# Optimization experiments

Measured on AMD Instinct MI355X. Metric: run time of the kernel, lower is better.

## Reference

```python
import jax, jax.numpy as jnp
import numpy as np

LMAX=4; MMAX=2; L2=25; M2=19; C=64; CE=64; NRBF=600; CUT=5.0
HEADS=8; ACH=32; VCH=16; HMSG=64; HFF=128; G=288; NL=2
AVG_NEI=20.0; AVG_NODES=2000.0
N_NODES=2000; N_EDGES=40000; NSPEC=90
# |m| group of each truncated (edge-frame) coefficient, order l=0..4, m=-min(l,2)..min(l,2)
MG = np.array([0, 1,0,1, 2,1,0,1,2, 2,1,0,1,2, 2,1,0,1,2])
# l of each full SH coefficient (25 total)
LOC = np.array([0] + [1]*3 + [2]*5 + [3]*7 + [4]*9)

def silu(x):
    return x * jax.nn.sigmoid(x)

def rms_norm_sh(x, w):
    # x: [N, 25, C]; w: [5, C] per-degree affine weight (rms_norm_sh)
    ms = jnp.mean(x * x, axis=1, keepdims=True)
    return x * jax.lax.rsqrt(ms + 1e-6) * w[LOC][None]

def setup_inputs() -> dict:
    key = jax.random.key(0)
    ks = iter(jax.random.split(key, 64))
    def rn(shape, scale):
        return jax.random.normal(next(ks), shape, dtype=jnp.float32) * scale
    inp = {}
    inp['edge_vectors'] = rn((N_EDGES, 3), 1.5)
    inp['wigner'] = rn((N_EDGES, M2, L2), 0.2)
    inp['wigner_inv'] = rn((N_EDGES, L2, M2), 0.2)
    inp['species_embed'] = rn((NSPEC, C), 1.0)
    inp['edge_species_embed'] = rn((NSPEC, 2 * CE), 1.0)
    DIN = NRBF + 2 * CE  # 728
    inp['deg_W1'] = rn((DIN, 128), DIN ** -0.5)
    inp['deg_b1'] = jnp.zeros((128,), jnp.float32)
    inp['deg_W2'] = rn((128, M2 * C), 128 ** -0.5)
    inp['deg_b2'] = jnp.zeros((M2 * C,), jnp.float32)
    inp['norm1_w'] = jnp.ones((NL, 5, C), jnp.float32)
    inp['rad_W1'] = rn((NL, DIN, 128), DIN ** -0.5)
    inp['rad_b1'] = jnp.zeros((NL, 128), jnp.float32)
    inp['rad_W2'] = rn((NL, 128, 3 * 2 * C), 128 ** -0.5)
    inp['rad_b2'] = jnp.ones((NL, 3 * 2 * C), jnp.float32)
    inp['so2_W'] = rn((NL, 3, 2 * C, HMSG), (2 * C) ** -0.5)
    inp['alpha_W'] = rn((NL, HMSG, HEADS * ACH), HMSG ** -0.5)
    inp['alpha_vec'] = rn((NL, HEADS, ACH), ACH ** -0.5)
    inp['value_W'] = rn((NL, 3, HMSG, HEADS * VCH), HMSG ** -0.5)
    inp['proj_W'] = rn((NL, 3, HEADS * VCH, C), (HEADS * VCH) ** -0.5)
    inp['norm2_w'] = jnp.ones((NL, 5, C), jnp.float32)
    inp['ffn_W1'] = rn((NL, C, HFF), C ** -0.5)
    inp['ffn_b1'] = jnp.zeros((NL, HFF), jnp.float32)
    inp['ffn_W2'] = rn((NL, HFF, C), HFF ** -0.5)
    inp['to_grid'] = rn((G, L2), L2 ** -0.5)
    inp['from_grid'] = rn((L2, G), G ** -0.5)
    inp['final_norm_w'] = jnp.ones((5, C), jnp.float32)
    inp['en_W1'] = rn((C, HFF), C ** -0.5)
    inp['en_b1'] = jnp.zeros((HFF,), jnp.float32)
    inp['en_W2'] = rn((HFF, 1), HFF ** -0.5)
    inp['en_b2'] = jnp.zeros((1,), jnp.float32)
    inp['node_species'] = jax.random.randint(next(ks), (N_NODES,), 0, NSPEC, dtype=jnp.int32)
    inp['senders'] = jax.random.randint(next(ks), (N_EDGES,), 0, N_NODES, dtype=jnp.int32)
    inp['receivers'] = jax.random.randint(next(ks), (N_EDGES,), 0, N_NODES, dtype=jnp.int32)
    inp['n_node'] = jnp.array([N_NODES], jnp.int32)
    return inp

def reference(edge_vectors, wigner, wigner_inv, species_embed, edge_species_embed,
              deg_W1, deg_b1, deg_W2, deg_b2, norm1_w, rad_W1, rad_b1, rad_W2, rad_b2,
              so2_W, alpha_W, alpha_vec, value_W, proj_W, norm2_w, ffn_W1, ffn_b1, ffn_W2,
              to_grid, from_grid, final_norm_w, en_W1, en_b1, en_W2, en_b2,
              node_species, senders, receivers, n_node):
    N = node_species.shape[0]
    E = senders.shape[0]
    mg = jnp.asarray(MG)
    # Gaussian RBF distance expansion (rbf_width=2.0)
    d = jnp.sqrt(jnp.sum(edge_vectors * edge_vectors, axis=-1) + 1e-12)
    offs = jnp.linspace(0.0, CUT, NRBF)
    std = 2.0 * (CUT / (NRBF - 1))
    rbf = jnp.exp(-0.5 * ((d[:, None] - offs[None, :]) / std) ** 2)  # [E, 600]
    # shared atom-edge embedding concat
    ne = edge_species_embed[node_species]
    se, re = jnp.split(ne, 2, axis=-1)
    ee = jnp.concatenate([rbf, se[senders], re[receivers]], axis=1)  # [E, 728]
    # initial node features: species embedding on l=0 component
    x = jnp.zeros((N, L2, C), dtype=edge_vectors.dtype).at[:, 0, :].set(species_embed[node_species])
    # edge degree embedding: radial MLP -> edge-frame coeffs -> rotate back -> scatter
    h = silu(ee @ deg_W1 + deg_b1) @ deg_W2 + deg_b2
    deg = jnp.einsum('elm,emc->elc', wigner_inv, h.reshape(E, M2, C))  # [E,25,C]
    x = x + jax.ops.segment_sum(deg, receivers, num_segments=N) / AVG_NEI
    for i in range(NL):
        # --- SO2 equivariant graph attention ---
        res = x
        xn = rms_norm_sh(x, norm1_w[i])
        msg = jnp.concatenate([xn[senders], xn[receivers]], axis=-1)      # [E,25,2C]
        msg = jnp.einsum('eml,elc->emc', wigner, msg)                     # rotate to edge frame [E,19,2C]
        rad = (silu(ee @ rad_W1[i] + rad_b1[i]) @ rad_W2[i] + rad_b2[i]).reshape(E, MMAX + 1, 2 * C)
        msg = msg * rad[:, mg]                                            # per-|m| radial modulation
        h = jnp.einsum('emc,mco->emo', msg, so2_W[i][mg])                 # SO2 conv [E,19,HMSG]
        a = (silu(h[:, 0, :]) @ alpha_W[i]).reshape(E, HEADS, ACH)        # invariant (m=0) alpha path
        logits = jnp.sum(silu(a) * alpha_vec[i][None], axis=-1)           # [E,HEADS]
        mx = jax.ops.segment_max(logits, receivers, num_segments=N)[receivers]
        ex = jnp.exp(logits - mx)
        den = jax.ops.segment_sum(ex, receivers, num_segments=N)[receivers]
        attn = ex / (den + 1e-12)
        v = jnp.einsum('emo,mov->emv', h, value_W[i][mg]).reshape(E, M2, HEADS, VCH)
        v = (v * attn[:, None, :, None]).reshape(E, M2, HEADS * VCH)
        oe = jnp.einsum('emv,mvc->emc', v, proj_W[i][mg])                 # [E,19,C]
        oe = jnp.einsum('elm,emc->elc', wigner_inv, oe)                   # rotate back [E,25,C]
        x = res + jax.ops.segment_sum(oe, receivers, num_segments=N)
        # --- S2 grid feed-forward ---
        res = x
        xn = rms_norm_sh(x, norm2_w[i])
        g = jnp.einsum('gl,nlc->ngc', to_grid, xn)                        # [N,288,C]
        g = silu(g @ ffn_W1[i] + ffn_b1[i]) @ ffn_W2[i]
        x = res + jnp.einsum('lg,ngc->nlc', from_grid, g)
    # final norm + energy head
    xn = rms_norm_sh(x, final_norm_w)
    g = jnp.einsum('gl,nlc->ngc', to_grid, xn)
    g = silu(g @ en_W1 + en_b1) @ en_W2 + en_b2
    eo = jnp.einsum('lg,ngo->nlo', from_grid, g)
    return eo[:, 0, 0] / AVG_NODES
```

## Files before the change

kernel.cpp:

```cpp
#include <hip/hip_runtime.h>
#include <hip/hip_bf16.h>
#include <math.h>


#define NRBF 600
#define DIN 728
#define GPTS 288

typedef __attribute__((ext_vector_type(8))) short bf16x8;
typedef __attribute__((ext_vector_type(4))) float f32x4;

__constant__ int d_mg[19] = {0,1,0,1,2,1,0,1,2,2,1,0,1,2,2,1,0,1,2};
__constant__ int d_loc[25] = {0,1,1,1,2,2,2,2,2,3,3,3,3,3,3,3,4,4,4,4,4,4,4,4,4};
__constant__ int d_mg0[5]={0,2,6,11,16};
__constant__ int d_mg1[8]={1,3,5,7,10,12,15,17};
__constant__ int d_mg2[6]={4,8,9,13,14,18};

__device__ inline float silu_f(float v){ return v/(1.0f+__expf(-v)); }
__device__ inline float bf2f(unsigned short u){ return __uint_as_float(((unsigned)u)<<16); }
__device__ inline unsigned short f2bf(float f){
  unsigned b=__float_as_uint(f);
  return (unsigned short)((b + 0x7FFF + ((b>>16)&1)) >> 16);
}

__device__ inline void atomicMaxF(float* addr, float val){
  int* ia=(int*)addr;
  int old=*ia;
  while (__int_as_float(old) < val){
    int assumed=old;
    old = atomicCAS(ia, assumed, __float_as_int(val));
    if (old == assumed) break;
  }
}

__global__ __launch_bounds__(256) void zero_cnt_kernel(int* cnt, int N){
  int i = blockIdx.x*256+threadIdx.x;
  if (i<N) cnt[i]=0;
}
__global__ __launch_bounds__(256) void csr_count_kernel(const int* __restrict__ rcv, int* cnt, int E){
  int i = blockIdx.x*256+threadIdx.x;
  if (i<E) atomicAdd(&cnt[rcv[i]],1);
}
__global__ __launch_bounds__(256) void csr_scan_kernel(const int* __restrict__ cnt,
    int* rowptr, int* fill, int N){
  __shared__ int s_part[256];
  int tid=threadIdx.x;
  int chunk=(N+255)/256;
  int lvals[12];
  int base=tid*chunk;
  int lsum=0;
  for (int i=0;i<chunk && i<12;i++){
    int v=(base+i<N)?cnt[base+i]:0;
    lvals[i]=lsum; lsum+=v;
  }
  s_part[tid]=lsum;
  __syncthreads();
  if (tid==0){
    int run=0;
    for (int t=0;t<256;t++){ int v=s_part[t]; s_part[t]=run; run+=v; }
  }
  __syncthreads();
  int off=s_part[tid];
  for (int i=0;i<chunk && i<12;i++){
    if (base+i<N){ rowptr[base+i]=off+lvals[i]; fill[base+i]=off+lvals[i]; }
  }
  if (tid==255) rowptr[N]=off+lsum;
}
__global__ __launch_bounds__(256) void csr_fill_kernel(const int* __restrict__ rcv,
    int* fill, int* eix, int E){
  int i = blockIdx.x*256+threadIdx.x;
  if (i<E){ int p=atomicAdd(&fill[rcv[i]],1); eix[p]=i; }
}

__global__ __launch_bounds__(256) void wsvb_kernel(const float* __restrict__ so2W,
    const float* __restrict__ valW, unsigned short* __restrict__ wsvb){
  int i=blockIdx.x/3, g=blockIdx.x%3;
  const float* A = so2W + (size_t)i*24576 + g*8192;
  const float* B = valW + (size_t)i*24576 + g*8192;
  unsigned short* C = wsvb + (size_t)blockIdx.x*16384;
  __shared__ float sB[8192];
  for (int j=threadIdx.x;j<2048;j+=256) ((float4*)sB)[j]=((const float4*)B)[j];
  __syncthreads();
  for (int idx=threadIdx.x; idx<16384; idx+=256){
    int k=idx>>7, j=idx&127;
    float acc=0;
    #pragma unroll 4
    for (int o=0;o<64;o++) acc += A[k*64+o]*sB[o*128+j];
    int pos = ((k>>5)*8 + (j>>4))*512 + (((k>>3)&3)*16 + (j&15))*8 + (k&7);
    C[pos]=f2bf(acc);
  }
}

__global__ __launch_bounds__(256) void projb_kernel(const float* __restrict__ pW,
    unsigned short* __restrict__ projb){
  const float* src = pW + (size_t)blockIdx.x*8192;
  unsigned short* dst = projb + (size_t)blockIdx.x*8192;
  for (int idx=threadIdx.x; idx<8192; idx+=256){
    int k=idx>>6, j=idx&63;
    int pos = ((k>>5)*4 + (j>>4))*512 + (((k>>3)&3)*16 + (j&15))*8 + (k&7);
    dst[pos]=f2bf(src[idx]);
  }
}

__global__ __launch_bounds__(256) void packB2g_kernel(const float* __restrict__ src,
    unsigned short* __restrict__ dh, unsigned short* __restrict__ dl, int K, int Nn){
  int ktiles=(K+31)>>5;
  int nnt=Nn>>4;
  int tot=ktiles*nnt*512;
  for (int idx=blockIdx.x*256+threadIdx.x; idx<tot; idx+=gridDim.x*256){
    int f=idx>>9, r=idx&511, lane=r>>3, j=r&7;
    int kt=f/nnt, nt=f-kt*nnt;
    int k=kt*32+(lane>>4)*8+j, c=nt*16+(lane&15);
    float v=(k<K)? src[k*Nn+c] : 0.0f;
    unsigned short h=f2bf(v);
    dh[idx]=h;
    dl[idx]=f2bf(v-bf2f(h));
  }
}

__global__ __launch_bounds__(256) void pack_tg2_kernel(const float* __restrict__ tg,
    unsigned short* __restrict__ tgp){
  int tid=threadIdx.x;
  for (int idx=tid; idx<9216; idx+=256){
    int t=idx>>9, r=idx&511, lane=r>>3, j=r&7;
    int kl=(lane>>4)*8+j, row=t*16+(lane&15);
    float v=(kl<25)? tg[row*25+kl] : 0.0f;
    unsigned short h=f2bf(v);
    tgp[idx]=h;
    tgp[9216+idx]=f2bf(v-bf2f(h));
  }
}

__global__ __launch_bounds__(256) void pack_fg2_kernel(const float* __restrict__ fg,
    unsigned short* __restrict__ fgp){
  int tid=threadIdx.x;
  for (int idx=tid; idx<18432; idx+=256){
    int f=idx>>9, r=idx&511, lane=r>>3, j=r&7;
    int t=f>>1, mt=f&1;
    int row=mt*16+(lane&15), k=(lane>>4)*8+j;
    float v=(row<25 && k<16)? fg[row*288+t*16+k] : 0.0f;
    unsigned short h=f2bf(v);
    fgp[idx]=h;
    fgp[18432+idx]=f2bf(v-bf2f(h));
  }
}

__global__ __launch_bounds__(256) void mlp_edge_kernel(const float* __restrict__ ev,
    const float* __restrict__ ese, const int* __restrict__ nsp,
    const unsigned short* __restrict__ w1h, const unsigned short* __restrict__ w1l,
    const float* __restrict__ b1,
    const unsigned short* __restrict__ w2h, const unsigned short* __restrict__ w2l,
    const float* __restrict__ b2,
    const int* __restrict__ snd, const int* __restrict__ rcv, const int* __restrict__ eix,
    int use_eix, int nt2, int mode,
    unsigned short* __restrict__ outb, float* __restrict__ outf, int E){
  int tid=threadIdx.x, wv=tid>>6, lane=tid&63;
  int lanelo=lane&15, khi=lane>>4;
  int p0=blockIdx.x*16;
  __shared__ unsigned short s_eeh[11776], s_eel[11776];
  __shared__ unsigned short s_h1h[2048], s_h1l[2048];
  __shared__ float s_d[16]; __shared__ int s_ss[16], s_rs[16];
  if (tid<16){
    int p=p0+tid;
    int e=(p<E)? (use_eix? eix[p] : p) : -1;
    if (e>=0){
      float vx=ev[3*e], vy=ev[3*e+1], vz=ev[3*e+2];
      s_d[tid]=sqrtf(vx*vx+vy*vy+vz*vz+1e-12f);
      s_ss[tid]=nsp[snd[e]]; s_rs[tid]=nsp[rcv[e]];
    } else { s_d[tid]=0.0f; s_ss[tid]=0; s_rs[tid]=0; }
  }
  __syncthreads();
  const float step=5.0f/599.0f, inv_std=1.0f/(2.0f*step);
  for (int idx=tid; idx<11776; idx+=256){
    int f=idx>>9, r=idx&511, ln=r>>3, j=r&7;
    int k=f*32+((ln>>4)<<3)+j, row=ln&15;
    float v=0.0f;
    if (k<NRBF){ float t=(s_d[row]-k*step)*inv_std; v=__expf(-0.5f*t*t); }
    else if (k<NRBF+64) v=ese[s_ss[row]*128+(k-NRBF)];
    else if (k<DIN)     v=ese[s_rs[row]*128+64+(k-NRBF-64)];
    unsigned short h=f2bf(v);
    s_eeh[idx]=h; s_eel[idx]=f2bf(v-bf2f(h));
  }
  __syncthreads();
  {
    f32x4 acc0={0,0,0,0}, acc1={0,0,0,0};
    int nta=wv*2, ntb=nta+1;
    for (int kt=0;kt<23;kt++){
      bf16x8 Ah=*(const bf16x8*)(s_eeh + kt*512 + lane*8);
      bf16x8 Al=*(const bf16x8*)(s_eel + kt*512 + lane*8);
      const unsigned short* bpa=w1h+(size_t)(kt*8+nta)*512+lane*8;
      const unsigned short* bpl=w1l+(size_t)(kt*8+nta)*512+lane*8;
      bf16x8 Bh=*(const bf16x8*)bpa;
      bf16x8 Bl=*(const bf16x8*)bpl;
      acc0=__builtin_amdgcn_mfma_f32_16x16x32_bf16(Ah,Bh,acc0,0,0,0);
      acc0=__builtin_amdgcn_mfma_f32_16x16x32_bf16(Al,Bh,acc0,0,0,0);
      acc0=__builtin_amdgcn_mfma_f32_16x16x32_bf16(Ah,Bl,acc0,0,0,0);
      bf16x8 Bh2=*(const bf16x8*)(bpa+512);
      bf16x8 Bl2=*(const bf16x8*)(bpl+512);
      acc1=__builtin_amdgcn_mfma_f32_16x16x32_bf16(Ah,Bh2,acc1,0,0,0);
      acc1=__builtin_amdgcn_mfma_f32_16x16x32_bf16(Al,Bh2,acc1,0,0,0);
      acc1=__builtin_amdgcn_mfma_f32_16x16x32_bf16(Ah,Bl2,acc1,0,0,0);
    }
    #pragma unroll
    for (int q=0;q<4;q++){
      int row=khi*4+q;
      {
        int col=nta*16+lanelo;
        float v=silu_f(acc0[q]+b1[col]);
        int pos=row*128 + (((col>>3)^(row&7))<<3) + (col&7);
        unsigned short h=f2bf(v);
        s_h1h[pos]=h; s_h1l[pos]=f2bf(v-bf2f(h));
      }
      {
        int col=ntb*16+lanelo;
        float v=silu_f(acc1[q]+b1[col]);
        int pos=row*128 + (((col>>3)^(row&7))<<3) + (col&7);
        unsigned short h=f2bf(v);
        s_h1h[pos]=h; s_h1l[pos]=f2bf(v-bf2f(h));
      }
    }
  }
  __syncthreads();
  bf16x8 Ahh[4],Ahl[4];
  #pragma unroll
  for (int kt=0;kt<4;kt++){
    int o=lanelo*128 + (((kt*4+khi)^(lanelo&7))<<3);
    Ahh[kt]=*(const bf16x8*)(s_h1h+o);
    Ahl[kt]=*(const bf16x8*)(s_h1l+o);
  }
  int ostride=nt2*16;
  for (int nt=wv; nt<nt2; nt+=4){
    f32x4 acc={0,0,0,0};
    #pragma unroll
    for (int kt=0;kt<4;kt++){
      const unsigned short* bp=w2h+(size_t)(kt*nt2+nt)*512+lane*8;
      bf16x8 Bh=*(const bf16x8*)bp;
      bf16x8 Bl=*(const bf16x8*)(w2l+(size_t)(kt*nt2+nt)*512+lane*8);
      acc=__builtin_amdgcn_mfma_f32_16x16x32_bf16(Ahh[kt],Bh,acc,0,0,0);
      acc=__builtin_amdgcn_mfma_f32_16x16x32_bf16(Ahl[kt],Bh,acc,0,0,0);
      acc=__builtin_amdgcn_mfma_f32_16x16x32_bf16(Ahh[kt],Bl,acc,0,0,0);
    }
    int col=nt*16+lanelo;
    float bb=b2[col];
    #pragma unroll
    for (int q=0;q<4;q++){
      int p=p0+khi*4+q;
      if (p<E){
        if (mode==0) outb[(size_t)p*ostride+col]=f2bf(acc[q]+bb);
        else         outf[(size_t)p*ostride+col]=acc[q]+bb;
      }
    }
  }
}

__global__ __launch_bounds__(256) void deg_sum_kernel(const unsigned short* __restrict__ h2,
    const float* __restrict__ winv, const int* __restrict__ rowptr, const int* __restrict__ eix,
    const int* __restrict__ nsp, const float* __restrict__ spe,
    float* __restrict__ x, int N){
  int n=blockIdx.x, tid=threadIdx.x;
  __shared__ float s_winv[475];
  __shared__ unsigned short s_oe[1216];
  int row0=rowptr[n];
  int cnt=rowptr[n+1]-row0;
  float4 acc0={0,0,0,0}, acc1={0,0,0,0};
  int it1=tid+256;
  for (int j=0;j<cnt;j++){
    int p=row0+j;
    int e=eix[p];
    for (int k2=tid;k2<475;k2+=256) s_winv[k2]=winv[(size_t)e*475+k2];
    for (int k2=tid;k2<152;k2+=256) ((int4*)s_oe)[k2]=((const int4*)(h2+(size_t)p*1216))[k2];
    __syncthreads();
    const unsigned* o2=(const unsigned*)s_oe;
    {
      int l=tid>>4, c4=tid&15;
      const float* wr=s_winv+l*19;
      #pragma unroll
      for (int m=0;m<19;m++){
        float w=wr[m];
        unsigned ua=o2[m*32+c4*2], ub=o2[m*32+c4*2+1];
        acc0.x+=w*bf2f((unsigned short)(ua&0xffffu));
        acc0.y+=w*bf2f((unsigned short)(ua>>16));
        acc0.z+=w*bf2f((unsigned short)(ub&0xffffu));
        acc0.w+=w*bf2f((unsigned short)(ub>>16));
      }
    }
    if (it1<400){
      int l=it1>>4, c4=it1&15;
      const float* wr=s_winv+l*19;
      #pragma unroll
      for (int m=0;m<19;m++){
        float w=wr[m];
        unsigned ua=o2[m*32+c4*2], ub=o2[m*32+c4*2+1];
        acc1.x+=w*bf2f((unsigned short)(ua&0xffffu));
        acc1.y+=w*bf2f((unsigned short)(ua>>16));
        acc1.z+=w*bf2f((unsigned short)(ub&0xffffu));
        acc1.w+=w*bf2f((unsigned short)(ub>>16));
      }
    }
    __syncthreads();
  }
  int sp=nsp[n];
  const float4* sp4=(const float4*)(spe+(size_t)sp*64);
  float4* xp=(float4*)(x+(size_t)n*1600);
  {
    int l=tid>>4, c4=tid&15;
    float4 base=(l==0)? sp4[c4] : make_float4(0,0,0,0);
    float4 o;
    o.x=base.x+0.05f*acc0.x; o.y=base.y+0.05f*acc0.y;
    o.z=base.z+0.05f*acc0.z; o.w=base.w+0.05f*acc0.w;
    xp[tid]=o;
  }
  if (it1<400){
    float4 o;
    o.x=0.05f*acc1.x; o.y=0.05f*acc1.y; o.z=0.05f*acc1.z; o.w=0.05f*acc1.w;
    xp[it1]=o;
  }
}

__global__ __launch_bounds__(256) void rmsnorm_kernel(const float* __restrict__ x,
    const float* __restrict__ w, float* __restrict__ xn, int N){
  int n = blockIdx.x, tid = threadIdx.x;
  __shared__ float s_x[1600];
  __shared__ float s_part[256];
  __shared__ float s_ms[64];
  const float* xr = x + (size_t)n*1600;
  for (int j=tid;j<1600;j+=256) s_x[j]=xr[j];
  __syncthreads();
  {
    int c = tid&63, seg = tid>>6;
    float acc=0;
    for (int l=seg;l<25;l+=4){ float v=s_x[l*64+c]; acc+=v*v; }
    s_part[tid]=acc;
  }
  __syncthreads();
  if (tid<64){
    float m=(s_part[tid]+s_part[tid+64]+s_part[tid+128]+s_part[tid+192])*(1.0f/25.0f);
    s_ms[tid]=rsqrtf(m+1e-6f);
  }
  __syncthreads();
  float* xo = xn + (size_t)n*1600;
  for (int j=tid;j<1600;j+=256){
    int l=j>>6, c=j&63;
    xo[j]=s_x[j]*s_ms[c]*w[d_loc[l]*64+c];
  }
}

__global__ __launch_bounds__(256) void init_mxden_kernel(float* mx, float* den, int N){
  int idx = blockIdx.x*256+threadIdx.x;
  if (idx < N*8){ mx[idx]=-3.0e38f; den[idx]=0.0f; }
}

__global__ __launch_bounds__(256) void logits_kernel(const float* __restrict__ xn,
    const float* __restrict__ wig, const float* __restrict__ radb,
    const float* __restrict__ so2W, const float* __restrict__ alphaW, const float* __restrict__ alphaV,
    const int* __restrict__ snd, const int* __restrict__ rcv,
    float* __restrict__ logits, float* __restrict__ mx, int E){
  int e = blockIdx.x, tid = threadIdx.x;
  __shared__ float s_cat[3200];
  __shared__ float s_wig0[25];
  __shared__ float s_msg0[128];
  __shared__ float s_sh0[64];
  __shared__ float s_a[256];
  int s = snd[e], r = rcv[e];
  const float4* xs4 = (const float4*)(xn + (size_t)s*1600);
  const float4* xr4 = (const float4*)(xn + (size_t)r*1600);
  float4* cat4 = (float4*)s_cat;
  for (int j=tid;j<400;j+=256){
    int l=j>>4, c4=j&15;
    cat4[l*32+c4]    = xs4[j];
    cat4[l*32+16+c4] = xr4[j];
  }
  if (tid<25) s_wig0[tid]=wig[(size_t)e*475+tid];
  __syncthreads();
  if (tid<128){
    float acc=0;
    #pragma unroll
    for (int l=0;l<25;l++) acc += s_wig0[l]*s_cat[l*128+tid];
    s_msg0[tid]=acc*radb[(size_t)e*384+tid];
  }
  __syncthreads();
  if (tid<64){
    float acc=0;
    #pragma unroll
    for (int k=0;k<128;k++) acc += s_msg0[k]*so2W[k*64+tid];
    s_sh0[tid]=silu_f(acc);
  }
  __syncthreads();
  {
    float acc=0;
    #pragma unroll
    for (int o=0;o<64;o++) acc += s_sh0[o]*alphaW[o*256+tid];
    s_a[tid]=silu_f(acc)*alphaV[tid];
  }
  __syncthreads();
  if (tid<8){
    float lg=0;
    #pragma unroll
    for (int q=0;q<32;q++) lg += s_a[tid*32+q];
    logits[(size_t)e*8+tid]=lg;
    atomicMaxF(&mx[r*8+tid], lg);
  }
}

__global__ __launch_bounds__(256) void den_kernel(const float* __restrict__ logits,
    const float* __restrict__ mx, const int* __restrict__ rcv,
    float* __restrict__ den, int E){
  int idx = blockIdx.x*256+threadIdx.x;
  if (idx >= E*8) return;
  int e = idx>>3, hd = idx&7, r = rcv[e];
  atomicAdd(&den[r*8+hd], __expf(logits[idx]-mx[r*8+hd]));
}

__global__ __launch_bounds__(256) void msg_kernel(const float* __restrict__ xn,
    const float* __restrict__ wig, const float* __restrict__ radb,
    const int* __restrict__ snd, const int* __restrict__ rcv, const int* __restrict__ eix,
    unsigned short* __restrict__ msgb, int E){
  __shared__ float s_wig[1900];
  int tid=threadIdx.x, wv=tid>>6, lane=tid&63;
  int p=blockIdx.x*4+wv;
  bool act=(p<E);
  int pc=act? p : (E-1);
  int e=eix[pc];
  int node=(lane<32)? snd[e] : rcv[e];
  int c2=(lane&31)*2;
  int col0=c2+((lane>>5)<<6);
  const float* xb=xn+(size_t)node*1600+c2;
  float ca[25], cb[25];
  #pragma unroll
  for (int l=0;l<25;l++){
    float2 v=*(const float2*)(xb+l*64);
    ca[l]=v.x; cb[l]=v.y;
  }
  float* swig=s_wig+wv*475;
  for (int j=lane;j<475;j+=64) swig[j]=wig[(size_t)e*475+j];
  float ra0,ra1,rb0,rb1,rc0,rc1;
  {
    const float* rb_=radb+(size_t)e*384;
    float2 v0=*(const float2*)(rb_+col0);
    float2 v1=*(const float2*)(rb_+128+col0);
    float2 v2=*(const float2*)(rb_+256+col0);
    ra0=v0.x; ra1=v0.y; rb0=v1.x; rb1=v1.y; rc0=v2.x; rc1=v2.y;
  }
  __syncthreads();
  unsigned short* dst=msgb+(size_t)pc*2432+col0;
  constexpr int mgc[19]={0,1,0,1,2,1,0,1,2,2,1,0,1,2,2,1,0,1,2};
  if (act){
    #pragma unroll
    for (int m=0;m<19;m++){
      float a0=0.0f,a1=0.0f;
      const float* wr=swig+m*25;
      #pragma unroll
      for (int l=0;l<25;l++){ float w=wr[l]; a0+=w*ca[l]; a1+=w*cb[l]; }
      float r0,r1;
      if (mgc[m]==0){ r0=ra0; r1=ra1; }
      else if (mgc[m]==1){ r0=rb0; r1=rb1; }
      else { r0=rc0; r1=rc1; }
      a0*=r0; a1*=r1;
      unsigned packv=((unsigned)f2bf(a1)<<16)|(unsigned)f2bf(a0);
      *(unsigned*)(dst+m*128)=packv;
    }
  }
}

__global__ __launch_bounds__(256) void attn_gemm_kernel(unsigned short* __restrict__ msgb,
    const unsigned short* __restrict__ wsvp, const unsigned short* __restrict__ projp,
    const float* __restrict__ logits, const float* __restrict__ mx, const float* __restrict__ den,
    const int* __restrict__ eix, const int* __restrict__ rcv, int E){
  int tid=threadIdx.x, wv=tid>>6, lane=tid&63;
  int lanelo=lane&15, khi=lane>>4;
  int p0=blockIdx.x*16;
  __shared__ unsigned short s_vv[2176];
  __shared__ float s_attn[16][8];
  __shared__ short s_r2e[304], s_r2m[304];
  for (int j=tid;j<304;j+=256){
    int e,m;
    if (j<80){ e=j/5; m=d_mg0[j%5]; }
    else if (j<208){ int q=j-80; e=q>>3; m=d_mg1[q&7]; }
    else { int q=j-208; e=q/6; m=d_mg2[q%6]; }
    s_r2e[j]=(short)e; s_r2m[j]=(short)m;
  }
  if (tid<128){
    int i=tid>>3, h=tid&7, p=p0+i;
    float a=0.0f;
    if (p<E){
      int e=eix[p]; int r=rcv[e];
      a=__expf(logits[(size_t)e*8+h]-mx[r*8+h])/(den[r*8+h]+1e-12f);
    }
    s_attn[i][h]=a;
  }
  __syncthreads();
  const int4* wp4=(const int4*)wsvp;
  const int4* pp4=(const int4*)projp;
  for (int t=0;t<19;t++){
    int g=(t<5)?0:((t<13)?1:2);
    int R=t*16+lanelo;
    int ei=s_r2e[R], mi=s_r2m[R];
    int pp=p0+ei;
    size_t abase=((size_t)((pp<E)?pp:0))*2432 + (size_t)mi*128;
    bf16x8 A[4];
    #pragma unroll
    for (int kt=0;kt<4;kt++)
      A[kt]=*(const bf16x8*)(msgb + abase + kt*32 + khi*8);
    #pragma unroll
    for (int h2=0;h2<2;h2++){
      int nt=wv*2+h2;
      f32x4 acc={0,0,0,0};
      #pragma unroll
      for (int kt=0;kt<4;kt++){
        int4 tt=wp4[g*2048+(kt*8+nt)*64+lane];
        acc=__builtin_amdgcn_mfma_f32_16x16x32_bf16(A[kt],*(bf16x8*)&tt,acc,0,0,0);
      }
      int col=nt*16+lanelo;
      #pragma unroll
      for (int q=0;q<4;q++){
        int r16=khi*4+q;
        int ei2=s_r2e[t*16+r16];
        s_vv[r16*136+col]=f2bf(acc[q]*s_attn[ei2][nt]);
      }
    }
    __syncthreads();
    {
      bf16x8 A2[4];
      #pragma unroll
      for (int kt=0;kt<4;kt++)
        A2[kt]=*(const bf16x8*)(s_vv + lanelo*136 + kt*32 + khi*8);
      f32x4 acc={0,0,0,0};
      #pragma unroll
      for (int kt=0;kt<4;kt++){
        int4 tt=pp4[g*1024+(kt*4+wv)*64+lane];
        acc=__builtin_amdgcn_mfma_f32_16x16x32_bf16(A2[kt],*(bf16x8*)&tt,acc,0,0,0);
      }
      int col=wv*16+lanelo;
      #pragma unroll
      for (int q=0;q<4;q++){
        int R2=t*16+khi*4+q;
        int pi=p0+s_r2e[R2];
        if (pi<E) msgb[(size_t)pi*2432 + (size_t)s_r2m[R2]*128 + col]=f2bf(acc[q]);
      }
    }
    __syncthreads();
  }
}

__global__ __launch_bounds__(256) void attn_sum_kernel(const unsigned short* __restrict__ msgb,
    const float* __restrict__ winv, const int* __restrict__ rowptr, const int* __restrict__ eix,
    float* __restrict__ x, int N){
  int n=blockIdx.x, tid=threadIdx.x;
  __shared__ float s_winv[475];
  __shared__ unsigned short s_oe[1216];
  int row0=rowptr[n];
  int cnt=rowptr[n+1]-row0;
  float4 acc0={0,0,0,0}, acc1={0,0,0,0};
  int it1=tid+256;
  for (int j=0;j<cnt;j++){
    int p=row0+j;
    int e=eix[p];
    for (int k2=tid;k2<475;k2+=256) s_winv[k2]=winv[(size_t)e*475+k2];
    for (int k2=tid;k2<152;k2+=256){
      int m=k2>>3, jj=k2&7;
      ((int4*)s_oe)[k2]=*(const int4*)(msgb + (size_t)p*2432 + m*128 + jj*8);
    }
    __syncthreads();
    const unsigned* o2=(const unsigned*)s_oe;
    {
      int l=tid>>4, c4=tid&15;
      const float* wr=s_winv+l*19;
      #pragma unroll
      for (int m=0;m<19;m++){
        float w=wr[m];
        unsigned ua=o2[m*32+c4*2], ub=o2[m*32+c4*2+1];
        acc0.x+=w*bf2f((unsigned short)(ua&0xffffu));
        acc0.y+=w*bf2f((unsigned short)(ua>>16));
        acc0.z+=w*bf2f((unsigned short)(ub&0xffffu));
        acc0.w+=w*bf2f((unsigned short)(ub>>16));
      }
    }
    if (it1<400){
      int l=it1>>4, c4=it1&15;
      const float* wr=s_winv+l*19;
      #pragma unroll
      for (int m=0;m<19;m++){
        float w=wr[m];
        unsigned ua=o2[m*32+c4*2], ub=o2[m*32+c4*2+1];
        acc1.x+=w*bf2f((unsigned short)(ua&0xffffu));
        acc1.y+=w*bf2f((unsigned short)(ua>>16));
        acc1.z+=w*bf2f((unsigned short)(ub&0xffffu));
        acc1.w+=w*bf2f((unsigned short)(ub>>16));
      }
    }
    __syncthreads();
  }
  float4* xp=(float4*)(x+(size_t)n*1600);
  {
    float4 c=xp[tid];
    c.x+=acc0.x; c.y+=acc0.y; c.z+=acc0.z; c.w+=acc0.w;
    xp[tid]=c;
  }
  if (it1<400){
    float4 c=xp[it1];
    c.x+=acc1.x; c.y+=acc1.y; c.z+=acc1.z; c.w+=acc1.w;
    xp[it1]=c;
  }
}

__global__ __launch_bounds__(256) void grid_ffn_mfma_kernel(const float* __restrict__ xn,
    const unsigned short* __restrict__ tgp, const unsigned short* __restrict__ fgp,
    const unsigned short* __restrict__ w1p, const unsigned short* __restrict__ w2p,
    const float* __restrict__ b1, float* __restrict__ x, int N){
  int n=blockIdx.x, tid=threadIdx.x, wv=tid>>6, lane=tid&63;
  int lanelo=lane&15, khi=lane>>4;
  __shared__ __align__(16) char s_mem[74240];
  unsigned short* s_w1=(unsigned short*)s_mem;
  unsigned short* s_xn=(unsigned short*)(s_mem+32768);
  float* s_b1=(float*)(s_mem+40960);
  unsigned short* scr=(unsigned short*)(s_mem+41472)+(size_t)wv*4096;
  for (int j=tid;j<2048;j+=256) ((int4*)s_w1)[j]=((const int4*)w1p)[j];
  if (tid<128) s_b1[tid]=b1[tid];
  { int4 z={0,0,0,0}; for (int j=tid;j<512;j+=256) ((int4*)s_xn)[j]=z; }
  __syncthreads();
  {
    const float* xr=xn+(size_t)n*1600;
    for (int j=tid;j<1600;j+=256){
      int k=j>>6, c=j&63;
      float v=xr[j];
      unsigned short h=f2bf(v);
      s_xn[c*32+k]=h;
      s_xn[2048+c*32+k]=f2bf(v-bf2f(h));
    }
  }
  __syncthreads();
  bf16x8 XBh[4],XBl[4];
  #pragma unroll
  for (int ct=0;ct<4;ct++){
    int o=(ct*16+lanelo)*32 + khi*8;
    XBh[ct]=*(const bf16x8*)(s_xn+o);
    XBl[ct]=*(const bf16x8*)(s_xn+2048+o);
  }
  f32x4 oacc[2][4];
  #pragma unroll
  for (int mt=0;mt<2;mt++)
    #pragma unroll
    for (int nt=0;nt<4;nt++){ f32x4 z={0,0,0,0}; oacc[mt][nt]=z; }
  for (int t=wv;t<18;t+=4){
    bf16x8 Atgh=*(const bf16x8*)(tgp + t*512 + lane*8);
    bf16x8 Atgl=*(const bf16x8*)(tgp + 9216 + t*512 + lane*8);
    #pragma unroll
    for (int ct=0;ct<4;ct++){
      f32x4 g={0,0,0,0};
      g=__builtin_amdgcn_mfma_f32_16x16x32_bf16(Atgh,XBh[ct],g,0,0,0);
      g=__builtin_amdgcn_mfma_f32_16x16x32_bf16(Atgl,XBh[ct],g,0,0,0);
      g=__builtin_amdgcn_mfma_f32_16x16x32_bf16(Atgh,XBl[ct],g,0,0,0);
      #pragma unroll
      for (int q=0;q<4;q++){
        int row=khi*4+q, col=ct*16+lanelo;
        int pos=row*64 + (((col>>3)^(row&7))<<3) + (col&7);
        float v=g[q]; unsigned short h=f2bf(v);
        scr[pos]=h; scr[1024+pos]=f2bf(v-bf2f(h));
      }
    }
    bf16x8 Agh[2],Agl[2];
    #pragma unroll
    for (int kt=0;kt<2;kt++){
      int o=lanelo*64 + (((kt*4+khi)^(lanelo&7))<<3);
      Agh[kt]=*(const bf16x8*)(scr+o);
      Agl[kt]=*(const bf16x8*)(scr+1024+o);
    }
    #pragma unroll
    for (int nt=0;nt<8;nt++){
      f32x4 h={0,0,0,0};
      #pragma unroll
      for (int kt=0;kt<2;kt++){
        bf16x8 Bh=*(const bf16x8*)(s_w1 + (kt*8+nt)*512 + lane*8);
        bf16x8 Bl=*(const bf16x8*)(s_w1 + 8192 + (kt*8+nt)*512 + lane*8);
        h=__builtin_amdgcn_mfma_f32_16x16x32_bf16(Agh[kt],Bh,h,0,0,0);
        h=__builtin_amdgcn_mfma_f32_16x16x32_bf16(Agl[kt],Bh,h,0,0,0);
        h=__builtin_amdgcn_mfma_f32_16x16x32_bf16(Agh[kt],Bl,h,0,0,0);
      }
      #pragma unroll
      for (int q=0;q<4;q++){
        int row=khi*4+q, col=nt*16+lanelo;
        float v=silu_f(h[q]+s_b1[col]);
        int pos=row*128 + (((col>>3)^(row&7))<<3) + (col&7);
        unsigned short hh=f2bf(v);
        scr[pos]=hh; scr[2048+pos]=f2bf(v-bf2f(hh));
      }
    }
    bf16x8 Ahh[4],Ahl[4];
    #pragma unroll
    for (int kt=0;kt<4;kt++){
      int o=lanelo*128 + (((kt*4+khi)^(lanelo&7))<<3);
      Ahh[kt]=*(const bf16x8*)(scr+o);
      Ahl[kt]=*(const bf16x8*)(scr+2048+o);
    }
    #pragma unroll
    for (int nt=0;nt<4;nt++){
      f32x4 o4={0,0,0,0};
      #pragma unroll
      for (int kt=0;kt<4;kt++){
        bf16x8 Bh=*(const bf16x8*)(w2p + (kt*4+nt)*512 + lane*8);
        bf16x8 Bl=*(const bf16x8*)(w2p + 8192 + (kt*4+nt)*512 + lane*8);
        o4=__builtin_amdgcn_mfma_f32_16x16x32_bf16(Ahh[kt],Bh,o4,0,0,0);
        o4=__builtin_amdgcn_mfma_f32_16x16x32_bf16(Ahl[kt],Bh,o4,0,0,0);
        o4=__builtin_amdgcn_mfma_f32_16x16x32_bf16(Ahh[kt],Bl,o4,0,0,0);
      }
      #pragma unroll
      for (int q=0;q<4;q++){
        int ch=nt*16+lanelo, rowk=khi*4+q;
        int pos=ch*32 + (((rowk>>3)^(ch&3))<<3) + (rowk&7);
        float v=o4[q]; unsigned short hh=f2bf(v);
        scr[pos]=hh; scr[2048+pos]=f2bf(v-bf2f(hh));
      }
    }
    bf16x8 Boh[4],Bol[4];
    #pragma unroll
    for (int nt=0;nt<4;nt++){
      int ch=nt*16+lanelo;
      int o=ch*32 + ((khi^(ch&3))<<3);
      Boh[nt]=*(const bf16x8*)(scr+o);
      Bol[nt]=*(const bf16x8*)(scr+2048+o);
    }
    #pragma unroll
    for (int mt=0;mt<2;mt++){
      bf16x8 Afh=*(const bf16x8*)(fgp + (t*2+mt)*512 + lane*8);
      bf16x8 Afl=*(const bf16x8*)(fgp + 18432 + (t*2+mt)*512 + lane*8);
      #pragma unroll
      for (int nt=0;nt<4;nt++){
        oacc[mt][nt]=__builtin_amdgcn_mfma_f32_16x16x32_bf16(Afh,Boh[nt],oacc[mt][nt],0,0,0);
        oacc[mt][nt]=__builtin_amdgcn_mfma_f32_16x16x32_bf16(Afl,Boh[nt],oacc[mt][nt],0,0,0);
        oacc[mt][nt]=__builtin_amdgcn_mfma_f32_16x16x32_bf16(Afh,Bol[nt],oacc[mt][nt],0,0,0);
      }
    }
  }
  __syncthreads();
  float* pout=(float*)s_mem;
  #pragma unroll
  for (int mt=0;mt<2;mt++)
    #pragma unroll
    for (int nt=0;nt<4;nt++)
      #pragma unroll
      for (int q=0;q<4;q++){
        int row=mt*16+khi*4+q, col=nt*16+lanelo;
        pout[wv*2048 + row*64 + col]=oacc[mt][nt][q];
      }
  __syncthreads();
  for (int j=tid;j<1600;j+=256)
    x[(size_t)n*1600+j] += pout[j]+pout[2048+j]+pout[4096+j]+pout[6144+j];
}

__global__ __launch_bounds__(256) void energy_mfma_kernel(const float* __restrict__ xn,
    const unsigned short* __restrict__ tgp, const float* __restrict__ fg,
    const unsigned short* __restrict__ enw1p, const float* __restrict__ b1,
    const float* __restrict__ w2, const float* __restrict__ b2,
    float* __restrict__ out, int N){
  int n=blockIdx.x, tid=threadIdx.x, wv=tid>>6, lane=tid&63;
  int lanelo=lane&15, khi=lane>>4;
  __shared__ __align__(16) char s_mem[59584];
  unsigned short* s_w1=(unsigned short*)s_mem;
  unsigned short* s_xn=(unsigned short*)(s_mem+32768);
  float* s_b1=(float*)(s_mem+40960);
  float* s_w2=(float*)(s_mem+41472);
  float* s_fg0=(float*)(s_mem+41984);
  float* s_red=(float*)(s_mem+43136);
  unsigned short* scr=(unsigned short*)(s_mem+43200)+(size_t)wv*2048;
  for (int j=tid;j<2048;j+=256) ((int4*)s_w1)[j]=((const int4*)enw1p)[j];
  if (tid<128){ s_b1[tid]=b1[tid]; s_w2[tid]=w2[tid]; }
  for (int j=tid;j<288;j+=256) s_fg0[j]=fg[j];
  { int4 z={0,0,0,0}; for (int j=tid;j<512;j+=256) ((int4*)s_xn)[j]=z; }
  __syncthreads();
  {
    const float* xr=xn+(size_t)n*1600;
    for (int j=tid;j<1600;j+=256){
      int k=j>>6, c=j&63;
      float v=xr[j];
      unsigned short h=f2bf(v);
      s_xn[c*32+k]=h;
      s_xn[2048+c*32+k]=f2bf(v-bf2f(h));
    }
  }
  __syncthreads();
  bf16x8 XBh[4],XBl[4];
  #pragma unroll
  for (int ct=0;ct<4;ct++){
    int o=(ct*16+lanelo)*32 + khi*8;
    XBh[ct]=*(const bf16x8*)(s_xn+o);
    XBl[ct]=*(const bf16x8*)(s_xn+2048+o);
  }
  float b2v=b2[0];
  float e=0.0f;
  for (int t=wv;t<18;t+=4){
    bf16x8 Atgh=*(const bf16x8*)(tgp + t*512 + lane*8);
    bf16x8 Atgl=*(const bf16x8*)(tgp + 9216 + t*512 + lane*8);
    #pragma unroll
    for (int ct=0;ct<4;ct++){
      f32x4 g={0,0,0,0};
      g=__builtin_amdgcn_mfma_f32_16x16x32_bf16(Atgh,XBh[ct],g,0,0,0);
      g=__builtin_amdgcn_mfma_f32_16x16x32_bf16(Atgl,XBh[ct],g,0,0,0);
      g=__builtin_amdgcn_mfma_f32_16x16x32_bf16(Atgh,XBl[ct],g,0,0,0);
      #pragma unroll
      for (int q=0;q<4;q++){
        int row=khi*4+q, col=ct*16+lanelo;
        int pos=row*64 + (((col>>3)^(row&7))<<3) + (col&7);
        float v=g[q]; unsigned short h=f2bf(v);
        scr[pos]=h; scr[1024+pos]=f2bf(v-bf2f(h));
      }
    }
    bf16x8 Agh[2],Agl[2];
    #pragma unroll
    for (int kt=0;kt<2;kt++){
      int o=lanelo*64 + (((kt*4+khi)^(lanelo&7))<<3);
      Agh[kt]=*(const bf16x8*)(scr+o);
      Agl[kt]=*(const bf16x8*)(scr+1024+o);
    }
    #pragma unroll
    for (int nt=0;nt<8;nt++){
      f32x4 h={0,0,0,0};
      #pragma unroll
      for (int kt=0;kt<2;kt++){
        bf16x8 Bh=*(const bf16x8*)(s_w1 + (kt*8+nt)*512 + lane*8);
        bf16x8 Bl=*(const bf16x8*)(s_w1 + 8192 + (kt*8+nt)*512 + lane*8);
        h=__builtin_amdgcn_mfma_f32_16x16x32_bf16(Agh[kt],Bh,h,0,0,0);
        h=__builtin_amdgcn_mfma_f32_16x16x32_bf16(Agl[kt],Bh,h,0,0,0);
        h=__builtin_amdgcn_mfma_f32_16x16x32_bf16(Agh[kt],Bl,h,0,0,0);
      }
      #pragma unroll
      for (int q=0;q<4;q++){
        int row=khi*4+q, col=nt*16+lanelo;
        float v=silu_f(h[q]+s_b1[col]);
        e += v*s_w2[col]*s_fg0[t*16+row];
      }
    }
    if (lanelo==0){
      #pragma unroll
      for (int q=0;q<4;q++) e += s_fg0[t*16+khi*4+q]*b2v;
    }
  }
  #pragma unroll
  for (int d=1;d<64;d<<=1) e += __shfl_xor(e,d);
  if (lane==0) s_red[wv]=e;
  __syncthreads();
  if (tid==0) out[n]=(s_red[0]+s_red[1]+s_red[2]+s_red[3])*(1.0f/2000.0f);
}

extern "C" void kernel_launch(void* const* d_in, const int* in_sizes, int n_in,
                              void* d_out, int out_size, void* d_ws, size_t ws_size,
                              hipStream_t stream){
  (void)n_in; (void)out_size; (void)ws_size;
  const float* ev   = (const float*)d_in[0];
  const float* wig  = (const float*)d_in[1];
  const float* winv = (const float*)d_in[2];
  const float* spe  = (const float*)d_in[3];
  const float* ese  = (const float*)d_in[4];
  const float* degW1= (const float*)d_in[5];
  const float* degb1= (const float*)d_in[6];
  const float* degW2= (const float*)d_in[7];
  const float* degb2= (const float*)d_in[8];
  const float* n1w  = (const float*)d_in[9];
  const float* radW1= (const float*)d_in[10];
  const float* radb1= (const float*)d_in[11];
  const float* radW2= (const float*)d_in[12];
  const float* radb2= (const float*)d_in[13];
  const float* so2W = (const float*)d_in[14];
  const float* aW   = (const float*)d_in[15];
  const float* aV   = (const float*)d_in[16];
  const float* vW   = (const float*)d_in[17];
  const float* pW   = (const float*)d_in[18];
  const float* n2w  = (const float*)d_in[19];
  const float* fW1  = (const float*)d_in[20];
  const float* fb1  = (const float*)d_in[21];
  const float* fW2  = (const float*)d_in[22];
  const float* tg   = (const float*)d_in[23];
  const float* fg   = (const float*)d_in[24];
  const float* fnw  = (const float*)d_in[25];
  const float* enW1 = (const float*)d_in[26];
  const float* enb1 = (const float*)d_in[27];
  const float* enW2 = (const float*)d_in[28];
  const float* enb2 = (const float*)d_in[29];
  const int* nsp = (const int*)d_in[30];
  const int* snd = (const int*)d_in[31];
  const int* rcv = (const int*)d_in[32];
  int N = in_sizes[30];
  int E = in_sizes[31];
  float* out = (float*)d_out;

  float* ws = (float*)d_ws;
  size_t off = 0;
  float* radbuf = ws + off; off += (size_t)E*384;
  float* logits = ws + off; off += (size_t)E*8;
  float* mx     = ws + off; off += (size_t)N*8;
  float* den    = ws + off; off += (size_t)N*8;
  float* x      = ws + off; off += (size_t)N*1600;
  float* xn     = ws + off; off += (size_t)N*1600;
  unsigned short* wsvb  = (unsigned short*)(ws + off); off += (size_t)6*16384/2;
  unsigned short* projb = (unsigned short*)(ws + off); off += (size_t)6*8192/2;
  int* cnt      = (int*)(ws + off); off += (size_t)N;
  int* rowptr   = (int*)(ws + off); off += (size_t)(N+1);
  int* fill     = (int*)(ws + off); off += (size_t)N;
  int* eixbuf   = (int*)(ws + off); off += (size_t)E;
  off = (off + 3) & ~((size_t)3);
  unsigned short* msgb  = (unsigned short*)(ws + off); off += (size_t)E*1216;
  unsigned short* tgp   = (unsigned short*)(ws + off); off += 9216;
  unsigned short* fgp   = (unsigned short*)(ws + off); off += 18432;
  unsigned short* wwp   = (unsigned short*)(ws + off); off += 32768;
  unsigned short* enw1p = (unsigned short*)(ws + off); off += 8192;
  unsigned short* degw1p = (unsigned short*)(ws + off); off += 94208;
  unsigned short* degw2p = (unsigned short*)(ws + off); off += 155648;
  unsigned short* radw1p = (unsigned short*)(ws + off); off += 94208*2;
  unsigned short* radw2p = (unsigned short*)(ws + off); off += 49152*2;

  zero_cnt_kernel<<<(N+255)/256, 256, 0, stream>>>(cnt, N);
  csr_count_kernel<<<(E+255)/256, 256, 0, stream>>>(rcv, cnt, E);
  csr_scan_kernel<<<1, 256, 0, stream>>>(cnt, rowptr, fill, N);
  csr_fill_kernel<<<(E+255)/256, 256, 0, stream>>>(rcv, fill, eixbuf, E);
  wsvb_kernel<<<6, 256, 0, stream>>>(so2W, vW, wsvb);
  projb_kernel<<<6, 256, 0, stream>>>(pW, projb);
  pack_tg2_kernel<<<1, 256, 0, stream>>>(tg, tgp);
  pack_fg2_kernel<<<1, 256, 0, stream>>>(fg, fgp);
  for (int i=0;i<2;i++){
    unsigned short* wl = wwp + (size_t)i*32768;
    packB2g_kernel<<<8, 256, 0, stream>>>(fW1 + (size_t)i*8192, wl, wl+8192, 64, 128);
    packB2g_kernel<<<8, 256, 0, stream>>>(fW2 + (size_t)i*8192, wl+16384, wl+24576, 128, 64);
  }
  packB2g_kernel<<<8, 256, 0, stream>>>(enW1, enw1p, enw1p+8192, 64, 128);
  packB2g_kernel<<<32, 256, 0, stream>>>(degW1, degw1p, degw1p+94208, DIN, 128);
  packB2g_kernel<<<32, 256, 0, stream>>>(degW2, degw2p, degw2p+155648, 128, 1216);
  for (int i=0;i<2;i++){
    unsigned short* r1 = radw1p + (size_t)i*188416;
    unsigned short* r2 = radw2p + (size_t)i*98304;
    packB2g_kernel<<<32, 256, 0, stream>>>(radW1 + (size_t)i*DIN*128, r1, r1+94208, DIN, 128);
    packB2g_kernel<<<16, 256, 0, stream>>>(radW2 + (size_t)i*128*384, r2, r2+49152, 128, 384);
  }

  mlp_edge_kernel<<<(E+15)/16, 256, 0, stream>>>(ev, ese, nsp,
      degw1p, degw1p+94208, degb1, degw2p, degw2p+155648, degb2,
      snd, rcv, eixbuf, 1, 76, 0, msgb, (float*)0, E);
  deg_sum_kernel<<<N, 256, 0, stream>>>(msgb, winv, rowptr, eixbuf, nsp, spe, x, N);

  for (int i=0;i<2;i++){
    rmsnorm_kernel<<<N, 256, 0, stream>>>(x, n1w + (size_t)i*320, xn, N);
    init_mxden_kernel<<<(N*8+255)/256, 256, 0, stream>>>(mx, den, N);
    {
      unsigned short* r1 = radw1p + (size_t)i*188416;
      unsigned short* r2 = radw2p + (size_t)i*98304;
      mlp_edge_kernel<<<(E+15)/16, 256, 0, stream>>>(ev, ese, nsp,
          r1, r1+94208, radb1 + (size_t)i*128, r2, r2+49152, radb2 + (size_t)i*384,
          snd, rcv, eixbuf, 0, 24, 1, (unsigned short*)0, radbuf, E);
    }
    logits_kernel<<<E, 256, 0, stream>>>(xn, wig, radbuf, so2W + (size_t)i*24576,
                                         aW + (size_t)i*64*256, aV + (size_t)i*256,
                                         snd, rcv, logits, mx, E);
    den_kernel<<<(E*8+255)/256, 256, 0, stream>>>(logits, mx, rcv, den, E);
    msg_kernel<<<(E+3)/4, 256, 0, stream>>>(xn, wig, radbuf, snd, rcv, eixbuf, msgb, E);
    attn_gemm_kernel<<<(E+15)/16, 256, 0, stream>>>(msgb,
                                                    wsvb + (size_t)i*3*16384, projb + (size_t)i*3*8192,
                                                    logits, mx, den, eixbuf, rcv, E);
    attn_sum_kernel<<<N, 256, 0, stream>>>(msgb, winv, rowptr, eixbuf, x, N);
    rmsnorm_kernel<<<N, 256, 0, stream>>>(x, n2w + (size_t)i*320, xn, N);
    grid_ffn_mfma_kernel<<<N, 256, 0, stream>>>(xn, tgp, fgp,
                                                wwp + (size_t)i*32768, wwp + (size_t)i*32768 + 16384,
                                                fb1 + (size_t)i*128, x, N);
  }
  rmsnorm_kernel<<<N, 256, 0, stream>>>(x, fnw, xn, N);
  energy_mfma_kernel<<<N, 256, 0, stream>>>(xn, tgp, fg, enw1p, enb1, enW2, enb2, out, N);
}
```

Before: 2.985 ms.

## Fuse degree and layer-0 radial MLPs sharing one edge-feature build

Merges the degree-embedding MLP and the layer-0 radial MLP into one kernel that builds the RBF plus species edge features once and runs both first-layer GEMMs on them. The edge-feature staging is split into chunks of 8 k-tiles, which shrinks the shared-memory footprint and may raise occupancy. Radial outputs are now written through the edge permutation (eix) into edge-indexed positions, so the fused kernel can run in sorted order. This removes one recomputation of the 728-wide feature tile and one launch, at the cost of extra syncs per chunk and more live accumulators.

```diff
diff --git a/kernel.cpp b/kernel.cpp
--- a/kernel.cpp
+++ b/kernel.cpp
@@ -6,6 +6,7 @@
 #define NRBF 600
 #define DIN 728
 #define GPTS 288
+#define CH 8
 
 typedef __attribute__((ext_vector_type(8))) short bf16x8;
 typedef __attribute__((ext_vector_type(4))) float f32x4;
@@ -145,24 +146,29 @@
   }
 }
 
-__global__ __launch_bounds__(256) void mlp_edge_kernel(const float* __restrict__ ev,
+__global__ __launch_bounds__(256) void mlpf_kernel(const float* __restrict__ ev,
     const float* __restrict__ ese, const int* __restrict__ nsp,
-    const unsigned short* __restrict__ w1h, const unsigned short* __restrict__ w1l,
-    const float* __restrict__ b1,
-    const unsigned short* __restrict__ w2h, const unsigned short* __restrict__ w2l,
-    const float* __restrict__ b2,
+    const unsigned short* __restrict__ dw1h, const unsigned short* __restrict__ dw1l,
+    const float* __restrict__ db1,
+    const unsigned short* __restrict__ dw2h, const unsigned short* __restrict__ dw2l,
+    const float* __restrict__ db2,
+    const unsigned short* __restrict__ r1h, const unsigned short* __restrict__ r1l,
+    const float* __restrict__ rb1,
+    const unsigned short* __restrict__ r2h, const unsigned short* __restrict__ r2l,
+    const float* __restrict__ rb2,
     const int* __restrict__ snd, const int* __restrict__ rcv, const int* __restrict__ eix,
-    int use_eix, int nt2, int mode,
-    unsigned short* __restrict__ outb, float* __restrict__ outf, int E){
+    int do_deg,
+    unsigned short* __restrict__ degout, float* __restrict__ radout, int E){
   int tid=threadIdx.x, wv=tid>>6, lane=tid&63;
   int lanelo=lane&15, khi=lane>>4;
   int p0=blockIdx.x*16;
-  __shared__ unsigned short s_eeh[11776], s_eel[11776];
+  __shared__ unsigned short s_eeh[4096], s_eel[4096];
   __shared__ unsigned short s_h1h[2048], s_h1l[2048];
-  __shared__ float s_d[16]; __shared__ int s_ss[16], s_rs[16];
+  __shared__ float s_d[16]; __shared__ int s_ss[16], s_rs[16], s_e[16];
   if (tid<16){
     int p=p0+tid;
-    int e=(p<E)? (use_eix? eix[p] : p) : -1;
+    int e=(p<E)? eix[p] : -1;
+    s_e[tid]=e;
     if (e>=0){
       float vx=ev[3*e], vy=ev[3*e+1], vz=ev[3*e+2];
       s_d[tid]=sqrtf(vx*vx+vy*vy+vz*vz+1e-12f);
@@ -171,83 +177,121 @@
   }
   __syncthreads();
   const float step=5.0f/599.0f, inv_std=1.0f/(2.0f*step);
-  for (int idx=tid; idx<11776; idx+=256){
-    int f=idx>>9, r=idx&511, ln=r>>3, j=r&7;
-    int k=f*32+((ln>>4)<<3)+j, row=ln&15;
-    float v=0.0f;
-    if (k<NRBF){ float t=(s_d[row]-k*step)*inv_std; v=__expf(-0.5f*t*t); }
-    else if (k<NRBF+64) v=ese[s_ss[row]*128+(k-NRBF)];
-    else if (k<DIN)     v=ese[s_rs[row]*128+64+(k-NRBF-64)];
-    unsigned short h=f2bf(v);
-    s_eeh[idx]=h; s_eel[idx]=f2bf(v-bf2f(h));
-  }
-  __syncthreads();
-  {
-    f32x4 acc0={0,0,0,0}, acc1={0,0,0,0};
-    int nta=wv*2, ntb=nta+1;
-    for (int kt=0;kt<23;kt++){
-      bf16x8 Ah=*(const bf16x8*)(s_eeh + kt*512 + lane*8);
-      bf16x8 Al=*(const bf16x8*)(s_eel + kt*512 + lane*8);
-      const unsigned short* bpa=w1h+(size_t)(kt*8+nta)*512+lane*8;
-      const unsigned short* bpl=w1l+(size_t)(kt*8+nta)*512+lane*8;
-      bf16x8 Bh=*(const bf16x8*)bpa;
-      bf16x8 Bl=*(const bf16x8*)bpl;
-      acc0=__builtin_amdgcn_mfma_f32_16x16x32_bf16(Ah,Bh,acc0,0,0,0);
-      acc0=__builtin_amdgcn_mfma_f32_16x16x32_bf16(Al,Bh,acc0,0,0,0);
-      acc0=__builtin_amdgcn_mfma_f32_16x16x32_bf16(Ah,Bl,acc0,0,0,0);
-      bf16x8 Bh2=*(const bf16x8*)(bpa+512);
-      bf16x8 Bl2=*(const bf16x8*)(bpl+512);
-      acc1=__builtin_amdgcn_mfma_f32_16x16x32_bf16(Ah,Bh2,acc1,0,0,0);
-      acc1=__builtin_amdgcn_mfma_f32_16x16x32_bf16(Al,Bh2,acc1,0,0,0);
-      acc1=__builtin_amdgcn_mfma_f32_16x16x32_bf16(Ah,Bl2,acc1,0,0,0);
-    }
+  int nta=wv*2, ntb=nta+1;
+  f32x4 z4={0,0,0,0};
+  f32x4 aD0=z4,aD1=z4,aR0=z4,aR1=z4;
+  for (int c=0;c<23;c+=CH){
+    int ncur=23-c; if (ncur>CH) ncur=CH;
+    for (int idx=tid; idx<ncur*512; idx+=256){
+      int f=idx>>9, r=idx&511, ln=r>>3, j=r&7;
+      int k=(c+f)*32+((ln>>4)<<3)+j, row=ln&15;
+      float v=0.0f;
+      if (k<NRBF){ float t=(s_d[row]-k*step)*inv_std; v=__expf(-0.5f*t*t); }
+      else if (k<NRBF+64) v=ese[s_ss[row]*128+(k-NRBF)];
+      else if (k<DIN)     v=ese[s_rs[row]*128+64+(k-NRBF-64)];
+      unsigned short h=f2bf(v);
+      s_eeh[idx]=h; s_eel[idx]=f2bf(v-bf2f(h));
+    }
+    __syncthreads();
+    for (int f=0; f<ncur; f++){
+      int kt=c+f;
+      bf16x8 Ah=*(const bf16x8*)(s_eeh + f*512 + lane*8);
+      bf16x8 Al=*(const bf16x8*)(s_eel + f*512 + lane*8);
+      size_t ba=(size_t)(kt*8+nta)*512+lane*8;
+      {
+        bf16x8 Bh=*(const bf16x8*)(r1h+ba), Bl=*(const bf16x8*)(r1l+ba);
+        bf16x8 Bh2=*(const bf16x8*)(r1h+ba+512), Bl2=*(const bf16x8*)(r1l+ba+512);
+        aR0=__builtin_amdgcn_mfma_f32_16x16x32_bf16(Ah,Bh,aR0,0,0,0);
+        aR0=__builtin_amdgcn_mfma_f32_16x16x32_bf16(Al,Bh,aR0,0,0,0);
+        aR0=__builtin_amdgcn_mfma_f32_16x16x32_bf16(Ah,Bl,aR0,0,0,0);
+        aR1=__builtin_amdgcn_mfma_f32_16x16x32_bf16(Ah,Bh2,aR1,0,0,0);
+        aR1=__builtin_amdgcn_mfma_f32_16x16x32_bf16(Al,Bh2,aR1,0,0,0);
+        aR1=__builtin_amdgcn_mfma_f32_16x16x32_bf16(Ah,Bl2,aR1,0,0,0);
+      }
+      if (do_deg){
+        bf16x8 Bh=*(const bf16x8*)(dw1h+ba), Bl=*(const bf16x8*)(dw1l+ba);
+        bf16x8 Bh2=*(const bf16x8*)(dw1h+ba+512), Bl2=*(const bf16x8*)(dw1l+ba+512);
+        aD0=__builtin_amdgcn_mfma_f32_16x16x32_bf16(Ah,Bh,aD0,0,0,0);
+        aD0=__builtin_amdgcn_mfma_f32_16x16x32_bf16(Al,Bh,aD0,0,0,0);
+        aD0=__builtin_amdgcn_mfma_f32_16x16x32_bf16(Ah,Bl,aD0,0,0,0);
+        aD1=__builtin_amdgcn_mfma_f32_16x16x32_bf16(Ah,Bh2,aD1,0,0,0);
+        aD1=__builtin_amdgcn_mfma_f32_16x16x32_bf16(Al,Bh2,aD1,0,0,0);
+        aD1=__builtin_amdgcn_mfma_f32_16x16x32_bf16(Ah,Bl2,aD1,0,0,0);
+      }
+    }
+    __syncthreads();
+  }
+  int nmlp = do_deg ? 2 : 1;
+  #pragma unroll 1
+  for (int it=0; it<nmlp; it++){
+    int is_deg = (it==1);
+    f32x4 a0 = is_deg ? aD0 : aR0;
+    f32x4 a1 = is_deg ? aD1 : aR1;
+    const float* b1 = is_deg ? db1 : rb1;
     #pragma unroll
     for (int q=0;q<4;q++){
       int row=khi*4+q;
       {
         int col=nta*16+lanelo;
-        float v=silu_f(acc0[q]+b1[col]);
+        float v=silu_f(a0[q]+b1[col]);
         int pos=row*128 + (((col>>3)^(row&7))<<3) + (col&7);
         unsigned short h=f2bf(v);
         s_h1h[pos]=h; s_h1l[pos]=f2bf(v-bf2f(h));
       }
       {
         int col=ntb*16+lanelo;
-        float v=silu_f(acc1[q]+b1[col]);
+        float v=silu_f(a1[q]+b1[col]);
         int pos=row*128 + (((col>>3)^(row&7))<<3) + (col&7);
         unsigned short h=f2bf(v);
         s_h1h[pos]=h; s_h1l[pos]=f2bf(v-bf2f(h));
       }
     }
-  }
-  __syncthreads();
-  bf16x8 Ahh[4],Ahl[4];
-  #pragma unroll
-  for (int kt=0;kt<4;kt++){
-    int o=lanelo*128 + (((kt*4+khi)^(lanelo&7))<<3);
-    Ahh[kt]=*(const bf16x8*)(s_h1h+o);
-    Ahl[kt]=*(const bf16x8*)(s_h1l+o);
-  }
-  int ostride=nt2*16;
-  for (int nt=wv; nt<nt2; nt+=4){
-    f32x4 acc={0,0,0,0};
+    __syncthreads();
+    bf16x8 Ahh[4],Ahl[4];
     #pragma unroll
     for (int kt=0;kt<4;kt++){
-      const unsigned short* bp=w2h+(size_t)(kt*nt2+nt)*512+lane*8;
-      bf16x8 Bh=*(const bf16x8*)bp;
-      bf16x8 Bl=*(const bf16x8*)(w2l+(size_t)(kt*nt2+nt)*512+lane*8);
-      acc=__builtin_amdgcn_mfma_f32_16x16x32_bf16(Ahh[kt],Bh,acc,0,0,0);
-      acc=__builtin_amdgcn_mfma_f32_16x16x32_bf16(Ahl[kt],Bh,acc,0,0,0);
-      acc=__builtin_amdgcn_mfma_f32_16x16x32_bf16(Ahh[kt],Bl,acc,0,0,0);
-    }
-    int col=nt*16+lanelo;
-    float bb=b2[col];
-    #pragma unroll
-    for (int q=0;q<4;q++){
-      int p=p0+khi*4+q;
-      if (p<E){
-        if (mode==0) outb[(size_t)p*ostride+col]=f2bf(acc[q]+bb);
-        else         outf[(size_t)p*ostride+col]=acc[q]+bb;
+      int o=lanelo*128 + (((kt*4+khi)^(lanelo&7))<<3);
+      Ahh[kt]=*(const bf16x8*)(s_h1h+o);
+      Ahl[kt]=*(const bf16x8*)(s_h1l+o);
+    }
+    __syncthreads();
+    if (is_deg){
+      for (int nt=wv; nt<76; nt+=4){
+        f32x4 acc=z4;
+        #pragma unroll
+        for (int kt=0;kt<4;kt++){
+          size_t bo=(size_t)(kt*76+nt)*512+lane*8;
+          bf16x8 Bh=*(const bf16x8*)(dw2h+bo), Bl=*(const bf16x8*)(dw2l+bo);
+          acc=__builtin_amdgcn_mfma_f32_16x16x32_bf16(Ahh[kt],Bh,acc,0,0,0);
+          acc=__builtin_amdgcn_mfma_f32_16x16x32_bf16(Ahl[kt],Bh,acc,0,0,0);
+          acc=__builtin_amdgcn_mfma_f32_16x16x32_bf16(Ahh[kt],Bl,acc,0,0,0);
+        }
+        int col=nt*16+lanelo;
+        float bb=db2[col];
+        #pragma unroll
+        for (int q=0;q<4;q++){
+          int p=p0+khi*4+q;
+          if (p<E) degout[(size_t)p*1216+col]=f2bf(acc[q]+bb);
+        }
+      }
+    } else {
+      for (int nt=wv; nt<24; nt+=4){
+        f32x4 acc=z4;
+        #pragma unroll
+        for (int kt=0;kt<4;kt++){
+          size_t bo=(size_t)(kt*24+nt)*512+lane*8;
+          bf16x8 Bh=*(const bf16x8*)(r2h+bo), Bl=*(const bf16x8*)(r2l+bo);
+          acc=__builtin_amdgcn_mfma_f32_16x16x32_bf16(Ahh[kt],Bh,acc,0,0,0);
+          acc=__builtin_amdgcn_mfma_f32_16x16x32_bf16(Ahl[kt],Bh,acc,0,0,0);
+          acc=__builtin_amdgcn_mfma_f32_16x16x32_bf16(Ahh[kt],Bl,acc,0,0,0);
+        }
+        int col=nt*16+lanelo;
+        float bb=rb2[col];
+        #pragma unroll
+        for (int q=0;q<4;q++){
+          int e=s_e[khi*4+q];
+          if (e>=0) radout[(size_t)e*384+col]=acc[q]+bb;
+        }
       }
     }
   }
@@ -930,21 +974,25 @@
     packB2g_kernel<<<16, 256, 0, stream>>>(radW2 + (size_t)i*128*384, r2, r2+49152, 128, 384);
   }
 
-  mlp_edge_kernel<<<(E+15)/16, 256, 0, stream>>>(ev, ese, nsp,
+  mlpf_kernel<<<(E+15)/16, 256, 0, stream>>>(ev, ese, nsp,
       degw1p, degw1p+94208, degb1, degw2p, degw2p+155648, degb2,
-      snd, rcv, eixbuf, 1, 76, 0, msgb, (float*)0, E);
+      radw1p, radw1p+94208, radb1,
+      radw2p, radw2p+49152, radb2,
+      snd, rcv, eixbuf, 1, msgb, radbuf, E);
   deg_sum_kernel<<<N, 256, 0, stream>>>(msgb, winv, rowptr, eixbuf, nsp, spe, x, N);
 
   for (int i=0;i<2;i++){
+    if (i==1){
+      unsigned short* r1 = radw1p + (size_t)188416;
+      unsigned short* r2 = radw2p + (size_t)98304;
+      mlpf_kernel<<<(E+15)/16, 256, 0, stream>>>(ev, ese, nsp,
+          degw1p, degw1p+94208, degb1, degw2p, degw2p+155648, degb2,
+          r1, r1+94208, radb1+128,
+          r2, r2+49152, radb2+384,
+          snd, rcv, eixbuf, 0, msgb, radbuf, E);
+    }
     rmsnorm_kernel<<<N, 256, 0, stream>>>(x, n1w + (size_t)i*320, xn, N);
     init_mxden_kernel<<<(N*8+255)/256, 256, 0, stream>>>(mx, den, N);
-    {
-      unsigned short* r1 = radw1p + (size_t)i*188416;
-      unsigned short* r2 = radw2p + (size_t)i*98304;
-      mlp_edge_kernel<<<(E+15)/16, 256, 0, stream>>>(ev, ese, nsp,
-          r1, r1+94208, radb1 + (size_t)i*128, r2, r2+49152, radb2 + (size_t)i*384,
-          snd, rcv, eixbuf, 0, 24, 1, (unsigned short*)0, radbuf, E);
-    }
     logits_kernel<<<E, 256, 0, stream>>>(xn, wig, radbuf, so2W + (size_t)i*24576,
                                          aW + (size_t)i*64*256, aV + (size_t)i*256,
                                          snd, rcv, logits, mx, E);
```

After: 2.938 ms. About the same (-1.6%).
